# Performance work log

Hardware: AMD Instinct MI355X
Metric: run time of the kernel (lower is better)

Reference implementation:

```python
import jax, jax.numpy as jnp
import numpy as np

SEARCH_RANGE = 4  # max_displacement == pad in tfa CorrelationCost


def setup_inputs() -> dict:
    key = jax.random.key(0)
    k1, k2 = jax.random.split(key)
    B, C, H, W = 4, 128, 128, 256
    prv = jax.random.normal(k1, (B, C, H, W), dtype=jnp.float32)
    nxt = jax.random.normal(k2, (B, C, H, W), dtype=jnp.float32)
    return {"prv": prv, "nxt": nxt}


def reference(prv, nxt):
    """tfa CorrelationCost with kernel_size=1, stride_1=stride_2=1,
    max_displacement=pad=SEARCH_RANGE, channels_first.

    out[b, k, y, x] = (1/C) * sum_c prv[b,c,y,x] * nxt_pad[b,c,y+dy,x+dx]
    with k = (dy+d)*(2d+1) + (dx+d) (dy outer loop, dx inner, as in the
    tfa CUDA kernel), nxt zero-padded by d on each spatial side.
    """
    d = SEARCH_RANGE
    B, C, H, W = prv.shape
    nd = 2 * d + 1  # neighborhood width -> nd*nd output channels
    nxt_pad = jnp.pad(nxt, ((0, 0), (0, 0), (d, d), (d, d)))
    inv_c = jnp.float32(1.0 / C)
    outs = []
    # fixed small loop over (2d+1)^2 = 81 displacement offsets
    for dy in range(nd):
        for dx in range(nd):
            shifted = jax.lax.dynamic_slice(nxt_pad, (0, 0, dy, dx), (B, C, H, W))
            # reduce over channels: [B, H, W]
            outs.append(jnp.einsum('bchw,bchw->bhw', prv, shifted) * inv_c)
    return jnp.stack(outs, axis=1)  # [B, 81, H, W]
```

## Files before the change

### kernel.cpp

```cpp
#include <hip/hip_runtime.h>


#define SR 4
#define ND 9
#define BB 4
#define CC 128
#define HH 128
#define WW 256
#define HW (HH * WW)
#define PADW 264

typedef __fp16 h2 __attribute__((ext_vector_type(2)));

static __device__ __forceinline__ h2 pk(float lo, float hi) {
    return __builtin_amdgcn_cvt_pkrtz(lo, hi);
}
static __device__ __forceinline__ h2 as_h2(unsigned u) {
    union { unsigned u; h2 h; } v; v.u = u; return v.h;
}
static __device__ __forceinline__ unsigned as_u32(h2 h) {
    union { unsigned u; h2 h; } v; v.h = h; return v.u;
}

#define CFENCE asm volatile("" ::: "memory")

__global__ __launch_bounds__(128, 2) void costvol_kernel(
    const float* __restrict__ prv,
    const float* __restrict__ nxt,
    float* __restrict__ out)
{
    __shared__ unsigned lds[2][2][3][PADW];

    const int nwg  = gridDim.x;
    const int cpx  = nwg >> 3;
    const int orig = blockIdx.x;
    const int wid  = (orig & 7) * cpx + (orig >> 3);

    const int g  = wid % 3;
    const int r_ = wid / 3;
    const int yp = r_ & 63;
    const int b  = r_ >> 6;

    const int tid  = threadIdx.x;
    const int w    = tid >> 6;
    const int lane = tid & 63;
    const int x0   = lane << 2;
    const int y    = (yp << 1) + w;
    const int r0   = y + 3 * g - SR;

    bool vok[3];
    #pragma unroll
    for (int j = 0; j < 3; ++j)
        vok[j] = ((unsigned)(r0 + j) < (unsigned)HH);

    const float* pg = prv + (size_t)b * CC * HW + (size_t)y * WW + x0;
    const float* ng = nxt + (size_t)b * CC * HW + x0 + (ptrdiff_t)r0 * WW;

    if (lane < 12) {
        const int e  = lane >= 6;
        const int t  = lane - (e ? 6 : 0);
        const int bf = t & 1;
        const int j  = t >> 1;
        *reinterpret_cast<uint4*>(&lds[w][bf][j][e ? 260 : 0]) =
            make_uint4(0u, 0u, 0u, 0u);
    }

    float acc[3][ND][4];
    #pragma unroll
    for (int j = 0; j < 3; ++j)
        #pragma unroll
        for (int dx = 0; dx < ND; ++dx)
            #pragma unroll
            for (int px = 0; px < 4; ++px)
                acc[j][dx][px] = 0.f;

    #define LOADP(k, P0, P1, N) do { \
        const float* pp_ = pg + (size_t)(2 * (k)) * HW; \
        P0 = *reinterpret_cast<const float4*>(pp_); \
        P1 = *reinterpret_cast<const float4*>(pp_ + HW); \
        const float* nn_ = ng + (size_t)(2 * (k)) * HW; \
        _Pragma("unroll") \
        for (int j_ = 0; j_ < 3; ++j_) { \
            if (vok[j_]) { \
                N[j_][0] = *reinterpret_cast<const float4*>(nn_ + j_ * WW); \
                N[j_][1] = *reinterpret_cast<const float4*>(nn_ + j_ * WW + HW); \
            } else { \
                N[j_][0] = make_float4(0.f, 0.f, 0.f, 0.f); \
                N[j_][1] = make_float4(0.f, 0.f, 0.f, 0.f); \
            } \
        } } while (0)

    #define PKN(NH, N) do { \
        _Pragma("unroll") \
        for (int j_ = 0; j_ < 3; ++j_) { \
            NH[j_][0] = as_u32(pk(N[j_][0].x, N[j_][1].x)); \
            NH[j_][1] = as_u32(pk(N[j_][0].y, N[j_][1].y)); \
            NH[j_][2] = as_u32(pk(N[j_][0].z, N[j_][1].z)); \
            NH[j_][3] = as_u32(pk(N[j_][0].w, N[j_][1].w)); \
        } } while (0)

    #define STAGE(bf, NH) do { \
        _Pragma("unroll") \
        for (int j_ = 0; j_ < 3; ++j_) \
            *reinterpret_cast<uint4*>(&lds[w][bf][j_][4 + x0]) = \
                make_uint4(NH[j_][0], NH[j_][1], NH[j_][2], NH[j_][3]); \
        } while (0)

    float4 P0c, P1c, P0n, P1n, Nc[3][2], Nn[3][2];
    unsigned nhc[3][4], nhn[3][4];

    LOADP(0, P0c, P1c, Nc);
    PKN(nhc, Nc);
    STAGE(0, nhc);
    CFENCE;

    for (int k = 0; k < 64; ++k) {
        const int bf = k & 1;
        if (k < 63) LOADP(k + 1, P0n, P1n, Nn);

        h2 ph[4];
        ph[0] = pk(P0c.x, P1c.x); ph[1] = pk(P0c.y, P1c.y);
        ph[2] = pk(P0c.z, P1c.z); ph[3] = pk(P0c.w, P1c.w);

        #pragma unroll
        for (int j = 0; j < 3; ++j) {
            const uint4 wl = *reinterpret_cast<const uint4*>(&lds[w][bf][j][x0]);
            const uint4 wr = *reinterpret_cast<const uint4*>(&lds[w][bf][j][x0 + 8]);
            h2 n12[12];
            n12[0] = as_h2(wl.x); n12[1] = as_h2(wl.y);
            n12[2] = as_h2(wl.z); n12[3] = as_h2(wl.w);
            n12[4] = as_h2(nhc[j][0]); n12[5] = as_h2(nhc[j][1]);
            n12[6] = as_h2(nhc[j][2]); n12[7] = as_h2(nhc[j][3]);
            n12[8] = as_h2(wr.x); n12[9] = as_h2(wr.y);
            n12[10] = as_h2(wr.z); n12[11] = as_h2(wr.w);
            #pragma unroll
            for (int dx = 0; dx < ND; ++dx)
                #pragma unroll
                for (int px = 0; px < 4; ++px)
                    acc[j][dx][px] =
                        __builtin_amdgcn_fdot2(ph[px], n12[dx + px], acc[j][dx][px], false);
        }

        if (k < 63) {
            PKN(nhn, Nn);
            STAGE(bf ^ 1, nhn);
            CFENCE;
            P0c = P0n; P1c = P1n;
            #pragma unroll
            for (int j = 0; j < 3; ++j)
                #pragma unroll
                for (int i = 0; i < 4; ++i)
                    nhc[j][i] = nhn[j][i];
        }
    }

    const float invc = 1.0f / (float)CC;
    #pragma unroll
    for (int j = 0; j < 3; ++j) {
        const int dy = 3 * g + j;
        #pragma unroll
        for (int dx = 0; dx < ND; ++dx) {
            float* op = out + ((size_t)(b * 81 + dy * ND + dx) * HH + y) * WW + x0;
            *reinterpret_cast<float4*>(op) =
                make_float4(acc[j][dx][0] * invc, acc[j][dx][1] * invc,
                            acc[j][dx][2] * invc, acc[j][dx][3] * invc);
        }
    }
}

extern "C" void kernel_launch(void* const* d_in, const int* in_sizes, int n_in,
                              void* d_out, int out_size, void* d_ws, size_t ws_size,
                              hipStream_t stream) {
    const float* prv = (const float*)d_in[0];
    const float* nxt = (const float*)d_in[1];
    float* out = (float*)d_out;

    const int nblocks = BB * (HH / 2) * 3;
    costvol_kernel<<<nblocks, 128, 0, stream>>>(prv, nxt, out);
}
```

Before: 60.75 us.

## Split channel reduction across two wave pairs with LDS reduction

```diff
diff --git a/kernel.cpp b/kernel.cpp
--- a/kernel.cpp
+++ b/kernel.cpp
@@ -9,6 +9,7 @@
 #define WW 256
 #define HW (HH * WW)
 #define PADW 264
+#define RSTR 40
 
 typedef __fp16 h2 __attribute__((ext_vector_type(2)));
 
@@ -24,12 +25,12 @@
 
 #define CFENCE asm volatile("" ::: "memory")
 
-__global__ __launch_bounds__(128, 2) void costvol_kernel(
+__global__ __launch_bounds__(256, 3) void costvol_kernel(
     const float* __restrict__ prv,
     const float* __restrict__ nxt,
     float* __restrict__ out)
 {
-    __shared__ unsigned lds[2][2][3][PADW];
+    __shared__ unsigned shraw[4 * 2 * 3 * PADW];
 
     const int nwg  = gridDim.x;
     const int cpx  = nwg >> 3;
@@ -44,8 +45,10 @@
     const int tid  = threadIdx.x;
     const int w    = tid >> 6;
     const int lane = tid & 63;
+    const int ry   = w & 1;
+    const int ch   = w >> 1;
     const int x0   = lane << 2;
-    const int y    = (yp << 1) + w;
+    const int y    = (yp << 1) + ry;
     const int r0   = y + 3 * g - SR;
 
     bool vok[3];
@@ -53,17 +56,20 @@
     for (int j = 0; j < 3; ++j)
         vok[j] = ((unsigned)(r0 + j) < (unsigned)HH);
 
-    const float* pg = prv + (size_t)b * CC * HW + (size_t)y * WW + x0;
-    const float* ng = nxt + (size_t)b * CC * HW + x0 + (ptrdiff_t)r0 * WW;
+    unsigned* stg = shraw + w * (2 * 3 * PADW);
 
     if (lane < 12) {
-        const int e  = lane >= 6;
-        const int t  = lane - (e ? 6 : 0);
-        const int bf = t & 1;
-        const int j  = t >> 1;
-        *reinterpret_cast<uint4*>(&lds[w][bf][j][e ? 260 : 0]) =
+        const int e  = lane >= 6 ? 1 : 0;
+        const int q  = lane - 6 * e;
+        const int bf = q & 1;
+        const int j  = q >> 1;
+        *reinterpret_cast<uint4*>(stg + (bf * 3 + j) * PADW + (e ? 260 : 0)) =
             make_uint4(0u, 0u, 0u, 0u);
     }
+
+    const size_t cbase = (size_t)(b * CC + (ch << 6)) * HW;
+    const float* pg = prv + cbase + (size_t)y * WW + x0;
+    const float* ng = nxt + cbase + (ptrdiff_t)r0 * WW + x0;
 
     float acc[3][ND][4];
     #pragma unroll
@@ -102,7 +108,7 @@
     #define STAGE(bf, NH) do { \
         _Pragma("unroll") \
         for (int j_ = 0; j_ < 3; ++j_) \
-            *reinterpret_cast<uint4*>(&lds[w][bf][j_][4 + x0]) = \
+            *reinterpret_cast<uint4*>(stg + ((bf) * 3 + j_) * PADW + 4 + x0) = \
                 make_uint4(NH[j_][0], NH[j_][1], NH[j_][2], NH[j_][3]); \
         } while (0)
 
@@ -114,9 +120,9 @@
     STAGE(0, nhc);
     CFENCE;
 
-    for (int k = 0; k < 64; ++k) {
+    for (int k = 0; k < 32; ++k) {
         const int bf = k & 1;
-        if (k < 63) LOADP(k + 1, P0n, P1n, Nn);
+        if (k < 31) LOADP(k + 1, P0n, P1n, Nn);
 
         h2 ph[4];
         ph[0] = pk(P0c.x, P1c.x); ph[1] = pk(P0c.y, P1c.y);
@@ -124,8 +130,9 @@
 
         #pragma unroll
         for (int j = 0; j < 3; ++j) {
-            const uint4 wl = *reinterpret_cast<const uint4*>(&lds[w][bf][j][x0]);
-            const uint4 wr = *reinterpret_cast<const uint4*>(&lds[w][bf][j][x0 + 8]);
+            const unsigned* row = stg + (bf * 3 + j) * PADW;
+            const uint4 wl = *reinterpret_cast<const uint4*>(row + x0);
+            const uint4 wr = *reinterpret_cast<const uint4*>(row + x0 + 8);
             h2 n12[12];
             n12[0] = as_h2(wl.x); n12[1] = as_h2(wl.y);
             n12[2] = as_h2(wl.z); n12[3] = as_h2(wl.w);
@@ -141,7 +148,7 @@
                         __builtin_amdgcn_fdot2(ph[px], n12[dx + px], acc[j][dx][px], false);
         }
 
-        if (k < 63) {
+        if (k < 31) {
             PKN(nhn, Nn);
             STAGE(bf ^ 1, nhn);
             CFENCE;
@@ -153,17 +160,34 @@
                     nhc[j][i] = nhn[j][i];
         }
     }
+    #undef STAGE
+    #undef PKN
+    #undef LOADP
 
     const float invc = 1.0f / (float)CC;
     #pragma unroll
     for (int j = 0; j < 3; ++j) {
-        const int dy = 3 * g + j;
-        #pragma unroll
-        for (int dx = 0; dx < ND; ++dx) {
-            float* op = out + ((size_t)(b * 81 + dy * ND + dx) * HH + y) * WW + x0;
-            *reinterpret_cast<float4*>(op) =
-                make_float4(acc[j][dx][0] * invc, acc[j][dx][1] * invc,
-                            acc[j][dx][2] * invc, acc[j][dx][3] * invc);
+        __syncthreads();
+        if (ch == 1) {
+            float* red = reinterpret_cast<float*>(shraw) + ((ry << 6) + lane) * RSTR;
+            #pragma unroll
+            for (int dx = 0; dx < ND; ++dx)
+                *reinterpret_cast<float4*>(red + (dx << 2)) =
+                    make_float4(acc[j][dx][0], acc[j][dx][1],
+                                acc[j][dx][2], acc[j][dx][3]);
+        }
+        __syncthreads();
+        if (ch == 0) {
+            const float* red = reinterpret_cast<const float*>(shraw) + ((ry << 6) + lane) * RSTR;
+            const int dy = 3 * g + j;
+            #pragma unroll
+            for (int dx = 0; dx < ND; ++dx) {
+                const float4 t = *reinterpret_cast<const float4*>(red + (dx << 2));
+                float* op = out + ((size_t)(b * 81 + dy * ND + dx) * HH + y) * WW + x0;
+                *reinterpret_cast<float4*>(op) = make_float4(
+                    (acc[j][dx][0] + t.x) * invc, (acc[j][dx][1] + t.y) * invc,
+                    (acc[j][dx][2] + t.z) * invc, (acc[j][dx][3] + t.w) * invc);
+            }
         }
     }
 }
@@ -176,5 +200,5 @@
     float* out = (float*)d_out;
 
     const int nblocks = BB * (HH / 2) * 3;
-    costvol_kernel<<<nblocks, 128, 0, stream>>>(prv, nxt, out);
-}
+    costvol_kernel<<<nblocks, 256, 0, stream>>>(prv, nxt, out);
+}
```

After: 50.75 us (median of 3 runs). 1.2x faster.
